# Kernel optimization log

Measured on AMD Instinct MI355X. Metric: run time of the kernel, lower is better.

Reference implementation:

```python
import jax, jax.numpy as jnp
import numpy as np
from jax import lax

# norse LIFParameters defaults: dt=1e-3, tau_mem_inv=100, tau_syn_inv=200, v_leak=0, v_reset=0
ALPHA = 100.0
DT_TM = 0.1   # dt * tau_mem_inv
DT_TS = 0.2   # dt * tau_syn_inv

@jax.custom_vjp
def superspike(x):
    # Heaviside forward, SuperSpike surrogate gradient backward
    return (x > 0).astype(x.dtype)

def _ss_fwd(x):
    return superspike(x), x

def _ss_bwd(x, g):
    return (g / (ALPHA * jnp.abs(x) + 1.0) ** 2,)

superspike.defvjp(_ss_fwd, _ss_bwd)

def lif_step(inp, v, i, v_th):
    # norse lif_feed_forward_step (feedforward LIF cell)
    v_dec = v + DT_TM * (i - v)           # v_leak = 0
    i_dec = i * (1.0 - DT_TS)
    z = superspike(v_dec - v_th)
    v_new = (1.0 - z) * v_dec             # reset to v_reset = 0 on spike
    return z, v_new, i_dec + inp

def conv2d(x, w):
    return lax.conv_general_dilated(x, w, (1, 1), 'VALID',
                                    dimension_numbers=('NCHW', 'OIHW', 'NCHW'))

def avg_pool2(x):
    s = lax.reduce_window(x, jnp.zeros((), x.dtype), lax.add,
                          (1, 1, 2, 2), (1, 1, 2, 2), 'VALID')
    return s * jnp.asarray(0.25, x.dtype)

def setup_inputs() -> dict:
    key = jax.random.key(0)
    ks = jax.random.split(key, 6)
    x = jax.random.uniform(ks[0], (40, 256, 1, 28, 28), dtype=jnp.float32)
    # kaiming-ish scales (1/sqrt(fan_in))
    w_conv1 = jax.random.normal(ks[1], (20, 1, 3, 3), jnp.float32) * (1.0 / np.sqrt(9))
    w_conv2 = jax.random.normal(ks[2], (50, 20, 3, 3), jnp.float32) * (1.0 / np.sqrt(180))
    w_fc1 = jax.random.normal(ks[3], (500, 6050), jnp.float32) * (1.0 / np.sqrt(6050))
    w_fc2 = jax.random.normal(ks[4], (200, 500), jnp.float32) * (1.0 / np.sqrt(500))
    w_fc_out = jax.random.normal(ks[5], (10, 200), jnp.float32) * (1.0 / np.sqrt(200))
    return {"x": x, "w_conv1": w_conv1, "w_conv2": w_conv2,
            "w_fc1": w_fc1, "w_fc2": w_fc2, "w_fc_out": w_fc_out}

def reference(x, w_conv1, w_conv2, w_fc1, w_fc2, w_fc_out):
    T, B = x.shape[0], x.shape[1]
    dt = x.dtype
    z0 = jnp.zeros((B, 20, 26, 26), dt)
    z1 = jnp.zeros((B, 50, 11, 11), dt)
    z2 = jnp.zeros((B, 500), dt)
    z3 = jnp.zeros((B, 200), dt)
    zo = jnp.zeros((B, 10), dt)
    carry0 = (z0, z0, z1, z1, z2, z2, z3, z3, zo, zo)

    def step(carry, xt):
        v0, i0, v1, i1, v2, i2, v3, i3, vo, io = carry
        z = conv2d(xt, w_conv1)
        z, v0, i0 = lif_step(z, v0, i0, 0.2)
        z = avg_pool2(z)
        z = conv2d(z, w_conv2)
        z, v1, i1 = lif_step(z, v1, i1, 0.2)
        z = z.reshape(B, -1)                      # [B, 50*11*11]
        z = z @ w_fc1.T
        z, v2, i2 = lif_step(z, v2, i2, 0.1)
        z = z @ w_fc2.T
        z, v3, i3 = lif_step(z, v3, i3, 0.05)
        z = z @ w_fc_out.T
        # LICell (norse li_feed_forward_step): output is decayed membrane voltage
        v_dec = vo + DT_TM * (io - vo)
        i_new = io * (1.0 - DT_TS) + z
        return (v0, i0, v1, i1, v2, i2, v3, i3, v_dec, i_new), v_dec

    _, voltages = lax.scan(step, carry0, x)
    return voltages  # [T, B, output_neurons]
```

## Files before the change

### kernel.cpp

```cpp
#include <hip/hip_runtime.h>
#include <hip/hip_bf16.h>

typedef _Float16 f16x8 __attribute__((ext_vector_type(8)));
typedef float f32x4  __attribute__((ext_vector_type(4)));
typedef unsigned short u16x4 __attribute__((ext_vector_type(4)));

#define T_STEPS 40
#define BATCH   256
#define S2LO    0.000244140625f

__device__ __forceinline__ unsigned short f2h_bits(float f) {
    union { _Float16 h; unsigned short u; } c; c.h = (_Float16)f; return c.u;
}

__device__ __forceinline__ float lif_update(float inp, float& v, float& i, float vth) {
    float vd = __fadd_rn(v, __fmul_rn(0.1f, __fsub_rn(i, v)));
    float id = __fmul_rn(0.8f, i);
    float z  = (vd > vth) ? 1.0f : 0.0f;
    v = (vd > vth) ? 0.0f : vd;
    i = __fadd_rn(id, inp);
    return z;
}

__device__ __forceinline__ void llds16(const unsigned short* g, void* l) {
    __builtin_amdgcn_global_load_lds(
        (const __attribute__((address_space(1))) unsigned int*)g,
        (__attribute__((address_space(3))) unsigned int*)l, 16, 0, 0);
}

__global__ __launch_bounds__(512) void k_conv1(
    const float* __restrict__ x,
    const float* __restrict__ w1,
    unsigned char* __restrict__ s0)
{
    const int b    = blockIdx.y;
    const int tid  = threadIdx.x;
    const int cell = blockIdx.x*512 + tid;
    const bool active = cell < 3380;
    const int pos  = cell / 20;
    const int oc   = cell % 20;
    const int pr   = pos / 13, q = pos % 13;
    const int r0   = 2*pr, c0 = 2*q;

    __shared__ __align__(16) float xl[2][784];

    float wr[9];
    if (active) {
        #pragma unroll
        for (int j = 0; j < 9; ++j) wr[j] = w1[oc*9 + j];
    }
    float vs[2][2], is[2][2];
    #pragma unroll
    for (int dr = 0; dr < 2; ++dr)
        #pragma unroll
        for (int dc = 0; dc < 2; ++dc) { vs[dr][dc] = 0.f; is[dr][dc] = 0.f; }

    if (tid < 196) {
        const float4* xs4 = (const float4*)(x + (size_t)b*784);
        *(float4*)&xl[0][tid*4] = xs4[tid];
    }

    for (int t = 0; t < T_STEPS; ++t) {
        __syncthreads();
        if (t + 1 < T_STEPS && tid < 196) {
            const float4* xs4 = (const float4*)(x + (size_t)((t+1)*BATCH + b)*784);
            *(float4*)&xl[(t+1)&1][tid*4] = xs4[tid];
        }
        const float* xc = xl[t&1];
        size_t base = (size_t)(t*BATCH + b) * 4096;

        if (active) {
            float tle[4][4];
            #pragma unroll
            for (int r = 0; r < 4; ++r)
                #pragma unroll
                for (int c = 0; c < 4; ++c)
                    tle[r][c] = xc[(r0 + r)*28 + c0 + c];
            int zsum = 0;
            #pragma unroll
            for (int dr = 0; dr < 2; ++dr)
                #pragma unroll
                for (int dc = 0; dc < 2; ++dc) {
                    float acc = 0.f;
                    #pragma unroll
                    for (int kr = 0; kr < 3; ++kr)
                        #pragma unroll
                        for (int kc = 0; kc < 3; ++kc)
                            acc += tle[dr+kr][dc+kc] * wr[kr*3+kc];
                    float z = lif_update(acc, vs[dr][dc], is[dr][dc], 0.2f);
                    zsum += (z > 0.5f) ? 1 : 0;
                }
            s0[base + (size_t)pos*24 + oc] = (unsigned char)zsum;
        } else {
            int p2 = cell - 3380;
            for (int idx = p2; idx < 716; idx += 204) {
                if (idx < 676) s0[base + (size_t)(idx >> 2)*24 + 20 + (idx & 3)] = 0;
                else           s0[base + 4056 + (idx - 676)] = 0;
            }
        }
    }
}

__global__ __launch_bounds__(256, 2) void k_conv2(
    const unsigned char* __restrict__ s0,
    const float* __restrict__ w2,
    unsigned short* __restrict__ z1)
{
    const int b    = blockIdx.x >> 1;
    const int half = blockIdx.x & 1;
    const int tid  = threadIdx.x;
    const int wv   = tid >> 6;
    const int lane = tid & 63;
    const int l15  = lane & 15;
    const int kg   = lane >> 4;
    const int wm   = wv;

    __shared__ __align__(16) unsigned short w2h[32*232];
    __shared__ __align__(16) unsigned short w2m[32*232];
    __shared__ __align__(16) unsigned short sIn[2*4096];

    for (int s = tid; s < 32*232; s += 256) {
        int ocw = s / 232, kk = s % 232;
        int g = kk / 24, ic = kk % 24;
        int oc = half*32 + ocw;
        float val = 0.f;
        if (oc < 50 && g < 9 && ic < 20) val = w2[(oc*20 + ic)*9 + g];
        _Float16 h = (_Float16)val;
        float r1 = (val - (float)h) * 4096.0f;
        union { _Float16 h; unsigned short u; } ch, cm;
        ch.h = h; cm.h = (_Float16)r1;
        w2h[s] = ch.u;
        w2m[s] = cm.u;
    }

    f16x8 bfrH[2][7];
    int addrA[2][7];
    #pragma unroll
    for (int mt = 0; mt < 2; ++mt) {
        int pos = wm*32 + mt*16 + l15;
        #pragma unroll
        for (int kt = 0; kt < 7; ++kt) {
            int k = kt*32 + kg*8;
            int g = k / 24, o = k - g*24;
            if (pos <= 120 && g <= 8) {
                int in_idx = pos + 2*(pos/11) + 13*(g/3) + (g % 3);
                addrA[mt][kt] = in_idx*48 + o*2;
            } else addrA[mt][kt] = 8128;
        }
    }

    {
        const unsigned char* srow = s0 + (size_t)(0*BATCH + b)*4096;
        uint4 raw = *(const uint4*)(srow + tid*16);
        unsigned short hv[16];
        #pragma unroll
        for (int w = 0; w < 4; ++w) {
            unsigned int u = ((const unsigned int*)&raw)[w];
            #pragma unroll
            for (int j = 0; j < 4; ++j)
                hv[w*4+j] = f2h_bits(0.25f * (float)((u >> (8*j)) & 0xFFu));
        }
        unsigned short* dst = sIn + tid*16;
        *(f16x8*)dst       = *(const f16x8*)&hv[0];
        *(f16x8*)(dst + 8) = *(const f16x8*)&hv[8];
    }
    __syncthreads();

    #pragma unroll
    for (int nt = 0; nt < 2; ++nt) {
        int n = nt*16 + l15;
        #pragma unroll
        for (int kt = 0; kt < 7; ++kt)
            bfrH[nt][kt] = *(const f16x8*)&w2h[n*232 + kt*32 + kg*8];
    }

    float vst[2][2][4], ist[2][2][4];
    #pragma unroll
    for (int mt = 0; mt < 2; ++mt)
        #pragma unroll
        for (int nt = 0; nt < 2; ++nt)
            #pragma unroll
            for (int r = 0; r < 4; ++r) { vst[mt][nt][r] = 0.f; ist[mt][nt][r] = 0.f; }

    const f32x4 zero4 = {0.f, 0.f, 0.f, 0.f};

    for (int t = 0; t < T_STEPS; ++t) {
        if (t > 0) __syncthreads();

        uint4 raw;
        if (t + 1 < T_STEPS)
            raw = *(const uint4*)(s0 + (size_t)((t+1)*BATCH + b)*4096 + tid*16);

        const char* curB = (const char*)(sIn + (t&1)*4096);

        f32x4 acch[2][2], accl[2][2];
        #pragma unroll
        for (int mt = 0; mt < 2; ++mt)
            #pragma unroll
            for (int nt = 0; nt < 2; ++nt) { acch[mt][nt] = zero4; accl[mt][nt] = zero4; }

        #pragma unroll
        for (int kt = 0; kt < 7; ++kt) {
            f16x8 bm[2];
            #pragma unroll
            for (int nt = 0; nt < 2; ++nt) {
                int n = nt*16 + l15, k = kt*32 + kg*8;
                bm[nt] = *(const f16x8*)&w2m[n*232 + k];
            }
            #pragma unroll
            for (int mt = 0; mt < 2; ++mt) {
                f16x8 a = *(const f16x8*)(curB + addrA[mt][kt]);
                #pragma unroll
                for (int nt = 0; nt < 2; ++nt) {
                    acch[mt][nt] = __builtin_amdgcn_mfma_f32_16x16x32_f16(
                        a, bfrH[nt][kt], acch[mt][nt], 0, 0, 0);
                    accl[mt][nt] = __builtin_amdgcn_mfma_f32_16x16x32_f16(
                        a, bm[nt], accl[mt][nt], 0, 0, 0);
                }
            }
        }

        size_t rowoff = (size_t)(t*BATCH + b) * 6208;
        #pragma unroll
        for (int mt = 0; mt < 2; ++mt) {
            int posb = wm*32 + mt*16 + kg*4;
            #pragma unroll
            for (int nt = 0; nt < 2; ++nt) {
                int ocn = half*32 + nt*16 + l15;
                u16x4 pack;
                #pragma unroll
                for (int r = 0; r < 4; ++r) {
                    float inp = __fadd_rn(acch[mt][nt][r], __fmul_rn(S2LO, accl[mt][nt][r]));
                    float z = lif_update(inp, vst[mt][nt][r], ist[mt][nt][r], 0.2f);
                    int pos = posb + r;
                    pack[r] = (pos <= 120 && z > 0.5f) ? (unsigned short)0x3C00 : (unsigned short)0;
                }
                if (ocn < 50 && posb < 121)
                    *(u16x4*)(z1 + rowoff + ocn*124 + posb) = pack;
            }
        }
        if (half == 0 && tid < 8) z1[rowoff + 6200 + tid] = 0;

        if (t + 1 < T_STEPS) {
            unsigned short hv[16];
            #pragma unroll
            for (int w = 0; w < 4; ++w) {
                unsigned int u = ((const unsigned int*)&raw)[w];
                #pragma unroll
                for (int j = 0; j < 4; ++j)
                    hv[w*4+j] = f2h_bits(0.25f * (float)((u >> (8*j)) & 0xFFu));
            }
            unsigned short* dst = sIn + ((t+1)&1)*4096 + tid*16;
            *(f16x8*)dst       = *(const f16x8*)&hv[0];
            *(f16x8*)(dst + 8) = *(const f16x8*)&hv[8];
        }
    }
}

__global__ __launch_bounds__(256, 4) void k_gemm_fc1(
    const unsigned short* __restrict__ A,
    const unsigned short* __restrict__ Bhi,
    const unsigned short* __restrict__ Blo,
    float* __restrict__ P)
{
    __shared__ __align__(16) unsigned short As[128*64];
    __shared__ __align__(16) unsigned short Bh[64*64];
    __shared__ __align__(16) unsigned short Bl[64*64];

    const int tid  = threadIdx.x;
    const int lane = tid & 63;
    const int wv   = tid >> 6;
    const int wm   = wv & 1, wn = wv >> 1;
    const int l15  = lane & 15, kg = lane >> 4;
    const int mbase = blockIdx.x * 128;
    const int nbase = blockIdx.y * 64;
    const int kz    = blockIdx.z;
    const int kb0   = kz * 3136;
    const int kiters = 49 - kz;

    float* Pz = P + (size_t)kz * 5242880;

    const f32x4 zero4 = {0.f, 0.f, 0.f, 0.f};
    f32x4 acch[4][2], accl[4][2];
    #pragma unroll
    for (int mt = 0; mt < 4; ++mt)
        #pragma unroll
        for (int nt = 0; nt < 2; ++nt) { acch[mt][nt] = zero4; accl[mt][nt] = zero4; }

    const int rowA = tid >> 3;
    const int sw   = (((tid & 7) ^ (rowA & 7))) * 8;
    char* ldsA = (char*)As + (size_t)wv*1024;
    char* ldsH = (char*)Bh + (size_t)wv*1024;
    char* ldsL = (char*)Bl + (size_t)wv*1024;

    for (int ki = 0; ki < kiters; ++ki) {
        int kb = kb0 + ki * 64;
        #pragma unroll
        for (int c = 0; c < 4; ++c)
            llds16(A + (size_t)(mbase + c*32 + rowA)*6208 + kb + sw, ldsA + c*4096);
        #pragma unroll
        for (int c = 0; c < 2; ++c) {
            llds16(Bhi + (size_t)(nbase + c*32 + rowA)*6208 + kb + sw, ldsH + c*4096);
            llds16(Blo + (size_t)(nbase + c*32 + rowA)*6208 + kb + sw, ldsL + c*4096);
        }
        __syncthreads();
        #pragma unroll
        for (int kt = 0; kt < 2; ++kt) {
            f16x8 bh[2], bl[2], afv[4];
            #pragma unroll
            for (int nt = 0; nt < 2; ++nt) {
                int rb = wn*32 + nt*16 + l15;
                int ch = ((kt*4 + kg) ^ (rb & 7)) * 8;
                bh[nt] = *(const f16x8*)&Bh[rb*64 + ch];
                bl[nt] = *(const f16x8*)&Bl[rb*64 + ch];
            }
            #pragma unroll
            for (int mt = 0; mt < 4; ++mt) {
                int ra = wm*64 + mt*16 + l15;
                int ch = ((kt*4 + kg) ^ (ra & 7)) * 8;
                afv[mt] = *(const f16x8*)&As[ra*64 + ch];
            }
            #pragma unroll
            for (int mt = 0; mt < 4; ++mt)
                #pragma unroll
                for (int nt = 0; nt < 2; ++nt) {
                    acch[mt][nt] = __builtin_amdgcn_mfma_f32_16x16x32_f16(
                        afv[mt], bh[nt], acch[mt][nt], 0, 0, 0);
                    accl[mt][nt] = __builtin_amdgcn_mfma_f32_16x16x32_f16(
                        afv[mt], bl[nt], accl[mt][nt], 0, 0, 0);
                }
        }
        __syncthreads();
    }

    #pragma unroll
    for (int mt = 0; mt < 4; ++mt) {
        int m0 = mbase + wm*64 + mt*16 + kg*4;
        #pragma unroll
        for (int nt = 0; nt < 2; ++nt) {
            int n = nbase + wn*32 + nt*16 + l15;
            #pragma unroll
            for (int r = 0; r < 4; ++r) {
                float s = __fadd_rn(acch[mt][nt][r], __fmul_rn(S2LO, accl[mt][nt][r]));
                Pz[(size_t)(m0 + r)*512 + n] = s;
            }
        }
    }
}

__global__ __launch_bounds__(256, 3) void k_gemm(
    const unsigned short* __restrict__ A,
    const unsigned short* __restrict__ B0,
    float* __restrict__ C0,
    int Kp, int kiters, int ldc, int nstore,
    size_t strideB, size_t strideC)
{
    __shared__ __align__(16) unsigned short As[128*64];
    __shared__ __align__(16) unsigned short Bs[128*64];
    const unsigned short* B = B0 + (size_t)blockIdx.z * strideB;
    float* C = C0 + (size_t)blockIdx.z * strideC;

    const int tid  = threadIdx.x;
    const int lane = tid & 63;
    const int wv   = tid >> 6;
    const int wm   = wv & 1, wn = wv >> 1;
    const int l15  = lane & 15, kg = lane >> 4;
    const int mbase = blockIdx.x * 128;
    const int nbase = blockIdx.y * 128;

    const f32x4 zero4 = {0.f, 0.f, 0.f, 0.f};
    f32x4 acc[4][4];
    #pragma unroll
    for (int mt = 0; mt < 4; ++mt)
        #pragma unroll
        for (int nt = 0; nt < 4; ++nt) acc[mt][nt] = zero4;

    const int rowA = tid >> 3;
    const int sw   = (((tid & 7) ^ (rowA & 7))) * 8;
    char* ldsA = (char*)As + (size_t)wv*1024;
    char* ldsB = (char*)Bs + (size_t)wv*1024;

    for (int ki = 0; ki < kiters; ++ki) {
        int kb = ki * 64;
        #pragma unroll
        for (int c = 0; c < 4; ++c) {
            int row = c*32 + rowA;
            llds16(A + (size_t)(mbase + row)*Kp + kb + sw, ldsA + c*4096);
            llds16(B + (size_t)(nbase + row)*Kp + kb + sw, ldsB + c*4096);
        }
        __syncthreads();
        #pragma unroll
        for (int kt = 0; kt < 2; ++kt) {
            f16x8 bfv[4], afv[4];
            #pragma unroll
            for (int nt = 0; nt < 4; ++nt) {
                int rb = wn*64 + nt*16 + l15;
                int ch = ((kt*4 + kg) ^ (rb & 7)) * 8;
                bfv[nt] = *(const f16x8*)&Bs[rb*64 + ch];
            }
            #pragma unroll
            for (int mt = 0; mt < 4; ++mt) {
                int ra = wm*64 + mt*16 + l15;
                int ch = ((kt*4 + kg) ^ (ra & 7)) * 8;
                afv[mt] = *(const f16x8*)&As[ra*64 + ch];
            }
            #pragma unroll
            for (int mt = 0; mt < 4; ++mt)
                #pragma unroll
                for (int nt = 0; nt < 4; ++nt)
                    acc[mt][nt] = __builtin_amdgcn_mfma_f32_16x16x32_f16(
                        afv[mt], bfv[nt], acc[mt][nt], 0, 0, 0);
        }
        __syncthreads();
    }

    #pragma unroll
    for (int mt = 0; mt < 4; ++mt) {
        int m0 = mbase + wm*64 + mt*16 + kg*4;
        #pragma unroll
        for (int nt = 0; nt < 4; ++nt) {
            int n = nbase + wn*64 + nt*16 + l15;
            if (n < nstore) {
                #pragma unroll
                for (int r = 0; r < 4; ++r)
                    C[(size_t)(m0 + r)*ldc + n] = acc[mt][nt][r];
            }
        }
    }
}

__global__ void k_pack(const float* __restrict__ src,
                       unsigned short* __restrict__ hi, unsigned short* __restrict__ lo,
                       int N, int K, int Kp, int total) {
    int idx = blockIdx.x*256 + threadIdx.x;
    if (idx >= total) return;
    int n = idx / Kp, k = idx - n*Kp;
    float v = (n < N && k < K) ? src[n*K + k] : 0.f;
    _Float16 h = (_Float16)v;
    float r1 = (v - (float)h) * 4096.0f;
    union { _Float16 h; unsigned short u; } ch, cl;
    ch.h = h; cl.h = (_Float16)r1;
    hi[idx] = ch.u;
    lo[idx] = cl.u;
}

__global__ void k_pack_fc1(const float* __restrict__ src,
                           unsigned short* __restrict__ hi, unsigned short* __restrict__ lo,
                           int total) {
    int idx = blockIdx.x*256 + threadIdx.x;
    if (idx >= total) return;
    int n = idx / 6208, k = idx - n*6208;
    int oc = k / 124, pos = k - oc*124;
    float v = (n < 500 && oc < 50 && pos < 121) ? src[n*6050 + oc*121 + pos] : 0.f;
    _Float16 h = (_Float16)v;
    float r1 = (v - (float)h) * 4096.0f;
    union { _Float16 h; unsigned short u; } ch, cl;
    ch.h = h; cl.h = (_Float16)r1;
    hi[idx] = ch.u;
    lo[idx] = cl.u;
}

__global__ __launch_bounds__(512) void k_lif_scan(
    const float* __restrict__ c0, size_t pstride,
    unsigned short* __restrict__ zout,
    int ld, int nvalid, float vth, float pscale)
{
    int b = blockIdx.x;
    int n = threadIdx.x;
    float v = 0.f, cur = 0.f;
    for (int t = 0; t < T_STEPS; ++t) {
        size_t idx = (size_t)(t*BATCH + b)*ld + n;
        float s = __fadd_rn(c0[idx], __fmul_rn(pscale, c0[idx + pstride]));
        float z = lif_update(s, v, cur, vth);
        zout[idx] = (n < nvalid && z > 0.5f) ? (unsigned short)0x3C00 : (unsigned short)0;
    }
}

__global__ void k_li(const float* __restrict__ c0, size_t pstride, float* __restrict__ out) {
    int g = blockIdx.x*64 + threadIdx.x;
    if (g >= 2560) return;
    int b = g / 10, n = g - b*10;
    float vo = 0.f, io = 0.f;
    for (int t = 0; t < T_STEPS; ++t) {
        size_t idx = (size_t)(t*BATCH + b)*16 + n;
        float s = __fadd_rn(c0[idx], __fmul_rn(S2LO, c0[idx + pstride]));
        float vd = __fadd_rn(vo, __fmul_rn(0.1f, __fsub_rn(io, vo)));
        out[(size_t)(t*BATCH + b)*10 + n] = vd;
        io = __fadd_rn(__fmul_rn(0.8f, io), s);
        vo = vd;
    }
}

extern "C" void kernel_launch(void* const* d_in, const int* in_sizes, int n_in,
                              void* d_out, int out_size, void* d_ws, size_t ws_size,
                              hipStream_t stream) {
    (void)in_sizes; (void)n_in; (void)out_size; (void)ws_size;
    const float* x   = (const float*)d_in[0];
    const float* w1  = (const float*)d_in[1];
    const float* w2  = (const float*)d_in[2];
    const float* wf1 = (const float*)d_in[3];
    const float* wf2 = (const float*)d_in[4];
    const float* wfo = (const float*)d_in[5];
    char* ws = (char*)d_ws;

    unsigned short* z1    = (unsigned short*)(ws);
    unsigned char*  s0    = (unsigned char*)(ws + 127139840);
    unsigned short* W1hi  = (unsigned short*)(ws + 127139840);
    unsigned short* W2hi  = (unsigned short*)(ws + 139853824);
    unsigned short* Wohi  = (unsigned short*)(ws + 140378112);
    float*          c2p   = (float*)(ws + 140509184);
    unsigned short* z2    = (unsigned short*)(ws);
    float*          c3p   = (float*)(ws + 10485760);
    unsigned short* z3    = (unsigned short*)(ws + 31457280);
    float*          c4p   = (float*)(ws + 36700160);

    k_conv1<<<dim3(7, 256), 512, 0, stream>>>(x, w1, s0);
    k_conv2<<<512, 256, 0, stream>>>(s0, w2, z1);

    k_pack_fc1<<<(3178496+255)/256, 256, 0, stream>>>(wf1, W1hi, W1hi+3178496, 3178496);
    k_pack<<<(131072+255)/256, 256, 0, stream>>>(wf2, W2hi, W2hi+131072, 200, 500, 512, 131072);
    k_pack<<<(32768+255)/256,  256, 0, stream>>>(wfo, Wohi, Wohi+32768,  10,  200, 256, 32768);

    k_gemm_fc1<<<dim3(80, 8, 2), 256, 0, stream>>>(z1, W1hi, W1hi+3178496, c2p);
    k_lif_scan<<<256, 512, 0, stream>>>(c2p, (size_t)5242880, z2, 512, 500, 0.1f, 1.0f);
    k_gemm<<<dim3(80,2,2), 256, 0, stream>>>(z2, W2hi, c3p, 512, 8, 256, 256,
                                             (size_t)131072, (size_t)2621440);
    k_lif_scan<<<256, 256, 0, stream>>>(c3p, (size_t)2621440, z3, 256, 200, 0.05f, S2LO);
    k_gemm<<<dim3(80,1,2), 256, 0, stream>>>(z3, Wohi, c4p, 256, 4, 16, 16,
                                             (size_t)32768, (size_t)163840);
    k_li<<<40, 64, 0, stream>>>(c4p, (size_t)163840, (float*)d_out);
}
```

Measured before the change: 408.4 us.

## Remap fc1 GEMM block order, merge weight packing kernels, prefetch scan inputs

The fc1 GEMM grid is flattened to 1D, and block IDs are remapped so that consecutive blocks on each XCD-strided group share M tiles, which should improve L2 reuse of the A operand across the 8 chiplets. The three weight-packing kernels are merged into one launch to cut launch overhead. The LIF and LI scan kernels are unrolled by four with a register prefetch of future timestep inputs, so more loads are in flight per thread. The remapping assumes round-robin block dispatch across XCDs, and the extra branches in the merged pack kernel may diverge slightly at the boundaries between weight ranges.

```diff
diff --git a/kernel.cpp b/kernel.cpp
--- a/kernel.cpp
+++ b/kernel.cpp
@@ -272,9 +272,14 @@
     const int wv   = tid >> 6;
     const int wm   = wv & 1, wn = wv >> 1;
     const int l15  = lane & 15, kg = lane >> 4;
-    const int mbase = blockIdx.x * 128;
-    const int nbase = blockIdx.y * 64;
-    const int kz    = blockIdx.z;
+
+    const int bid   = blockIdx.x;
+    const int chunk = (bid & 7) * 160 + (bid >> 3);
+    const int mb    = chunk >> 4;
+    const int nn    = chunk & 15;
+    const int mbase = mb * 128;
+    const int nbase = (nn >> 1) * 64;
+    const int kz    = nn & 1;
     const int kb0   = kz * 3136;
     const int kiters = 49 - kz;
 
@@ -429,35 +434,36 @@
     }
 }
 
-__global__ void k_pack(const float* __restrict__ src,
-                       unsigned short* __restrict__ hi, unsigned short* __restrict__ lo,
-                       int N, int K, int Kp, int total) {
+__global__ void k_pack_all(
+    const float* __restrict__ wf1, const float* __restrict__ wf2,
+    const float* __restrict__ wfo,
+    unsigned short* __restrict__ W1, unsigned short* __restrict__ W2,
+    unsigned short* __restrict__ Wo)
+{
     int idx = blockIdx.x*256 + threadIdx.x;
-    if (idx >= total) return;
-    int n = idx / Kp, k = idx - n*Kp;
-    float v = (n < N && k < K) ? src[n*K + k] : 0.f;
+    float v; unsigned short *hi, *lo; int off;
+    if (idx < 3178496) {
+        int n = idx / 6208, k = idx - n*6208;
+        int oc = k / 124, pos = k - oc*124;
+        v = (n < 500 && oc < 50 && pos < 121) ? wf1[n*6050 + oc*121 + pos] : 0.f;
+        hi = W1; lo = W1 + 3178496; off = idx;
+    } else if (idx < 3178496 + 131072) {
+        int i2 = idx - 3178496;
+        int n = i2 >> 9, k = i2 & 511;
+        v = (n < 200 && k < 500) ? wf2[n*500 + k] : 0.f;
+        hi = W2; lo = W2 + 131072; off = i2;
+    } else if (idx < 3178496 + 131072 + 32768) {
+        int i3 = idx - 3178496 - 131072;
+        int n = i3 >> 8, k = i3 & 255;
+        v = (n < 10 && k < 200) ? wfo[n*200 + k] : 0.f;
+        hi = Wo; lo = Wo + 32768; off = i3;
+    } else return;
     _Float16 h = (_Float16)v;
     float r1 = (v - (float)h) * 4096.0f;
     union { _Float16 h; unsigned short u; } ch, cl;
     ch.h = h; cl.h = (_Float16)r1;
-    hi[idx] = ch.u;
-    lo[idx] = cl.u;
-}
-
-__global__ void k_pack_fc1(const float* __restrict__ src,
-                           unsigned short* __restrict__ hi, unsigned short* __restrict__ lo,
-                           int total) {
-    int idx = blockIdx.x*256 + threadIdx.x;
-    if (idx >= total) return;
-    int n = idx / 6208, k = idx - n*6208;
-    int oc = k / 124, pos = k - oc*124;
-    float v = (n < 500 && oc < 50 && pos < 121) ? src[n*6050 + oc*121 + pos] : 0.f;
-    _Float16 h = (_Float16)v;
-    float r1 = (v - (float)h) * 4096.0f;
-    union { _Float16 h; unsigned short u; } ch, cl;
-    ch.h = h; cl.h = (_Float16)r1;
-    hi[idx] = ch.u;
-    lo[idx] = cl.u;
+    hi[off] = ch.u;
+    lo[off] = cl.u;
 }
 
 __global__ __launch_bounds__(512) void k_lif_scan(
@@ -468,27 +474,70 @@
     int b = blockIdx.x;
     int n = threadIdx.x;
     float v = 0.f, cur = 0.f;
-    for (int t = 0; t < T_STEPS; ++t) {
-        size_t idx = (size_t)(t*BATCH + b)*ld + n;
-        float s = __fadd_rn(c0[idx], __fmul_rn(pscale, c0[idx + pstride]));
-        float z = lif_update(s, v, cur, vth);
-        zout[idx] = (n < nvalid && z > 0.5f) ? (unsigned short)0x3C00 : (unsigned short)0;
-    }
-}
-
-__global__ void k_li(const float* __restrict__ c0, size_t pstride, float* __restrict__ out) {
+    const float* sx = c0 + (size_t)b*ld + n;
+    const float* sy = sx + pstride;
+    const size_t step = (size_t)BATCH*ld;
+    float x0 = sx[0],      y0 = sy[0];
+    float x1 = sx[step],   y1 = sy[step];
+    float x2 = sx[2*step], y2 = sy[2*step];
+    float x3 = sx[3*step], y3 = sy[3*step];
+
+    #define LIF_SUB(J, XV, YV)                                                \
+        {                                                                     \
+            float s = __fadd_rn(XV, __fmul_rn(pscale, YV));                   \
+            float z = lif_update(s, v, cur, vth);                             \
+            zout[(size_t)((t+J)*BATCH + b)*ld + n] =                          \
+                (n < nvalid && z > 0.5f) ? (unsigned short)0x3C00             \
+                                         : (unsigned short)0;                 \
+            if (t + J + 4 < T_STEPS) {                                        \
+                XV = sx[(size_t)(t + J + 4)*step];                            \
+                YV = sy[(size_t)(t + J + 4)*step];                            \
+            }                                                                 \
+        }
+
+    for (int t = 0; t < T_STEPS; t += 4) {
+        LIF_SUB(0, x0, y0);
+        LIF_SUB(1, x1, y1);
+        LIF_SUB(2, x2, y2);
+        LIF_SUB(3, x3, y3);
+    }
+    #undef LIF_SUB
+}
+
+__global__ void k_li(const float* __restrict__ c0, size_t pstride,
+                     float* __restrict__ out) {
     int g = blockIdx.x*64 + threadIdx.x;
     if (g >= 2560) return;
     int b = g / 10, n = g - b*10;
+    const float* sx = c0 + (size_t)b*16 + n;
+    const float* sy = sx + pstride;
+    const size_t step = (size_t)BATCH*16;
     float vo = 0.f, io = 0.f;
-    for (int t = 0; t < T_STEPS; ++t) {
-        size_t idx = (size_t)(t*BATCH + b)*16 + n;
-        float s = __fadd_rn(c0[idx], __fmul_rn(S2LO, c0[idx + pstride]));
-        float vd = __fadd_rn(vo, __fmul_rn(0.1f, __fsub_rn(io, vo)));
-        out[(size_t)(t*BATCH + b)*10 + n] = vd;
-        io = __fadd_rn(__fmul_rn(0.8f, io), s);
-        vo = vd;
-    }
+    float x0 = sx[0],      y0 = sy[0];
+    float x1 = sx[step],   y1 = sy[step];
+    float x2 = sx[2*step], y2 = sy[2*step];
+    float x3 = sx[3*step], y3 = sy[3*step];
+
+    #define LI_SUB(J, XV, YV)                                                 \
+        {                                                                     \
+            float s = __fadd_rn(XV, __fmul_rn(S2LO, YV));                     \
+            float vd = __fadd_rn(vo, __fmul_rn(0.1f, __fsub_rn(io, vo)));     \
+            out[(size_t)((t+J)*BATCH + b)*10 + n] = vd;                       \
+            io = __fadd_rn(__fmul_rn(0.8f, io), s);                           \
+            vo = vd;                                                          \
+            if (t + J + 4 < T_STEPS) {                                        \
+                XV = sx[(size_t)(t + J + 4)*step];                            \
+                YV = sy[(size_t)(t + J + 4)*step];                            \
+            }                                                                 \
+        }
+
+    for (int t = 0; t < T_STEPS; t += 4) {
+        LI_SUB(0, x0, y0);
+        LI_SUB(1, x1, y1);
+        LI_SUB(2, x2, y2);
+        LI_SUB(3, x3, y3);
+    }
+    #undef LI_SUB
 }
 
 extern "C" void kernel_launch(void* const* d_in, const int* in_sizes, int n_in,
@@ -517,11 +566,10 @@
     k_conv1<<<dim3(7, 256), 512, 0, stream>>>(x, w1, s0);
     k_conv2<<<512, 256, 0, stream>>>(s0, w2, z1);
 
-    k_pack_fc1<<<(3178496+255)/256, 256, 0, stream>>>(wf1, W1hi, W1hi+3178496, 3178496);
-    k_pack<<<(131072+255)/256, 256, 0, stream>>>(wf2, W2hi, W2hi+131072, 200, 500, 512, 131072);
-    k_pack<<<(32768+255)/256,  256, 0, stream>>>(wfo, Wohi, Wohi+32768,  10,  200, 256, 32768);
-
-    k_gemm_fc1<<<dim3(80, 8, 2), 256, 0, stream>>>(z1, W1hi, W1hi+3178496, c2p);
+    k_pack_all<<<(3342336+255)/256, 256, 0, stream>>>(wf1, wf2, wfo,
+                                                      W1hi, W2hi, Wohi);
+
+    k_gemm_fc1<<<1280, 256, 0, stream>>>(z1, W1hi, W1hi+3178496, c2p);
     k_lif_scan<<<256, 512, 0, stream>>>(c2p, (size_t)5242880, z2, 512, 500, 0.1f, 1.0f);
     k_gemm<<<dim3(80,2,2), 256, 0, stream>>>(z2, W2hi, c3p, 512, 8, 256, 256,
                                              (size_t)131072, (size_t)2621440);
```

Result: no change. 407.3 us (-0.3%).
